# Kernel optimization log

Measured on AMD Instinct MI355X. Metric: run time of the kernel, lower is better.

The kernel has to match this reference:

```python
import jax, jax.numpy as jnp
import numpy as np

NFFT = 512
SHIFT = 160
EPS = 1e-07
LOG10 = float(np.log(10.0))


def setup_inputs() -> dict:
    key = jax.random.key(0)
    x = jax.random.normal(key, (32, 1, 96512), dtype=jnp.float32)
    n = np.arange(NFFT)
    ang = 2.0 * np.pi * np.outer(n, n) / NFFT  # [k, n]
    W_real = np.cos(ang).astype(np.float32)
    W_imag = (-np.sin(ang)).astype(np.float32)
    return {"x": x, "W_real": jnp.asarray(W_real), "W_imag": jnp.asarray(W_imag)}


def reference(x, W_real, W_imag):
    # x: [B, C, T]; W_real/W_imag: [nfft, nfft] DFT basis (kernel k over taps n)
    B, C, T = x.shape
    n_frames = (T - NFFT) // SHIFT + 1
    # strided frame extraction == Conv1d(stride=SHIFT, kernel=NFFT) unfolding
    idx = jnp.arange(n_frames)[:, None] * SHIFT + jnp.arange(NFFT)[None, :]  # [F, N]
    frames = x[:, :, idx]  # [B, C, F, N]
    real = jnp.einsum('bcfn,kn->bckf', frames, W_real)  # [B, C, nfft, F]
    imag = jnp.einsum('bcfn,kn->bckf', frames, W_imag)
    # mode == 'log': log10 of magnitude spectrogram (with epsilon inside sqrt)
    fft = jnp.log(jnp.sqrt(real * real + imag * imag + EPS)) / LOG10
    fft = fft[:, :, : NFFT // 2, :]  # keep lower half of spectrum
    # normalize_feature: zero-mean, unit-std over frequency axis (biased std)
    mean = jnp.mean(fft, axis=2, keepdims=True)
    std = jnp.std(fft, axis=2, keepdims=True)
    return (fft - mean) / (std + EPS)
```

## Files before the change

### kernel.cpp

```cpp
#include <hip/hip_runtime.h>
#include <stdint.h>

#define TLEN    96512
#define NBATCH  32
#define KOUT    256
#define SHIFT   160
#define NFRAMES 601
#define FT      76
#define NTILES  8
#define NKS     16
#define DEPTH   3
#define EPSF    1e-7f

typedef _Float16 f16;
typedef _Float16 half8 __attribute__((ext_vector_type(8)));
typedef float f32x16 __attribute__((ext_vector_type(16)));

#define SPAN       ((FT - 1) * SHIFT + 256)
#define UNITS      (SPAN / 8)
#define PLANE_B    24576
#define LDS_RED    104704
#define LDS_STAT   (LDS_RED + 6144)
#define LDS_TOTAL  (LDS_STAT + 768)

__global__ __launch_bounds__(256) void split_w_kernel(
    const float* __restrict__ Wr, const float* __restrict__ Wi,
    f16* __restrict__ wsW)
{
    int id = blockIdx.x * 256 + threadIdx.x;
    int n8 = id & 31;
    int k  = (id >> 5) & 255;
    int ri = (id >> 13) & 1;
    const float* src = (ri ? Wi : Wr) + k * 512 + n8 * 8;
    f16 h[8], l[8];
    #pragma unroll
    for (int j = 0; j < 8; ++j) {
        float v = src[j];
        h[j] = (f16)v;
        l[j] = (f16)(v - (float)h[j]);
    }
    int par = k & 1, kk = k >> 1;
    int l31 = kk & 31, J = kk >> 5;
    int ks  = n8 >> 1, lhi = n8 & 1;
    int c0  = ((par * 4 + J) * 16 + ks) * 4 + ri * 2;
    size_t off = (size_t)(l31 * 2 + lhi) * 8;
    *(half8*)(wsW + (size_t)(c0 + 0) * 512 + off) = *(half8*)h;
    *(half8*)(wsW + (size_t)(c0 + 1) * 512 + off) = *(half8*)l;
}

__device__ __forceinline__ void load_a(half8 (&a)[2][2],
    const f16* __restrict__ wsW, int par, int J, int laneoff, int ks)
{
    #pragma unroll
    for (int ri = 0; ri < 2; ++ri)
      #pragma unroll
      for (int hl = 0; hl < 2; ++hl) {
          int c = ((par * 4 + J) * 16 + ks) * 4 + ri * 2 + hl;
          a[ri][hl] = *(const half8*)(wsW + (size_t)c * 512 + laneoff);
      }
}

__device__ __forceinline__ void load_b(half8 (&bb)[3][2],
    const char* smem, int par, int l31, int lhi, int ks)
{
    #pragma unroll
    for (int nf = 0; nf < 3; ++nf)
      #pragma unroll
      for (int hl = 0; hl < 2; ++hl) {
          int u  = (nf * 32 + l31) * 20 + ks * 2 + lhi;
          int up = u ^ ((u >> 3) & 7);
          bb[nf][hl] = *(const half8*)(smem + (par * 2 + hl) * PLANE_B + up * 16);
      }
}

__device__ __forceinline__ void do_mfma(f32x16 (&acc)[3][2],
    const half8 (&a)[2][2], const half8 (&bb)[3][2])
{
    __builtin_amdgcn_s_setprio(1);
    #pragma unroll
    for (int nf = 0; nf < 3; ++nf)
      #pragma unroll
      for (int ri = 0; ri < 2; ++ri) {
          acc[nf][ri] = __builtin_amdgcn_mfma_f32_32x32x16_f16(
              a[ri][0], bb[nf][0], acc[nf][ri], 0, 0, 0);
          acc[nf][ri] = __builtin_amdgcn_mfma_f32_32x32x16_f16(
              a[ri][0], bb[nf][1], acc[nf][ri], 0, 0, 0);
          acc[nf][ri] = __builtin_amdgcn_mfma_f32_32x32x16_f16(
              a[ri][1], bb[nf][0], acc[nf][ri], 0, 0, 0);
      }
    __builtin_amdgcn_s_setprio(0);
}

__global__ __launch_bounds__(512, 2) void dft_mfma_kernel(
    const f16* __restrict__ wsW, const float* __restrict__ x,
    float* __restrict__ out)
{
    __shared__ uint4 smem4[LDS_TOTAL / 16];
    char* smem = (char*)smem4;

    const int tid  = threadIdx.x;
    const int lane = tid & 63;
    const int w    = tid >> 6;
    const int l31  = lane & 31;
    const int lhi  = lane >> 5;
    const int b    = blockIdx.y;
    const int f0   = blockIdx.x * FT;
    const int par  = w & 1;
    const int J    = w >> 1;
    const int laneoff = (l31 * 2 + lhi) * 8;

    half8 A[DEPTH][2][2];
    #pragma unroll
    for (int s = 0; s < DEPTH; ++s)
        load_a(A[s], wsW, par, J, laneoff, s);

    {
        const float* __restrict__ xb = x + (size_t)b * TLEN;
        const int t0 = f0 * SHIFT;
        for (int u = tid; u < UNITS; u += 512) {
            int t = t0 + u * 8;
            float va[8], vb[8];
            if (t + 264 <= TLEN) {
                float4 p0 = *(const float4*)(xb + t);
                float4 p1 = *(const float4*)(xb + t + 4);
                float4 q0 = *(const float4*)(xb + t + 256);
                float4 q1 = *(const float4*)(xb + t + 260);
                va[0]=p0.x; va[1]=p0.y; va[2]=p0.z; va[3]=p0.w;
                va[4]=p1.x; va[5]=p1.y; va[6]=p1.z; va[7]=p1.w;
                vb[0]=q0.x; vb[1]=q0.y; vb[2]=q0.z; vb[3]=q0.w;
                vb[4]=q1.x; vb[5]=q1.y; vb[6]=q1.z; vb[7]=q1.w;
            } else {
                #pragma unroll
                for (int j = 0; j < 8; ++j) {
                    int ta = t + j, tb = t + 256 + j;
                    va[j] = (ta < TLEN) ? xb[ta] : 0.f;
                    vb[j] = (tb < TLEN) ? xb[tb] : 0.f;
                }
            }
            f16 eh[8], el[8], oh[8], ol[8];
            #pragma unroll
            for (int j = 0; j < 8; ++j) {
                float E = va[j] + vb[j], O = va[j] - vb[j];
                eh[j] = (f16)E; el[j] = (f16)(E - (float)eh[j]);
                oh[j] = (f16)O; ol[j] = (f16)(O - (float)oh[j]);
            }
            int up = u ^ ((u >> 3) & 7);
            *(half8*)(smem + 0 * PLANE_B + up * 16) = *(half8*)eh;
            *(half8*)(smem + 1 * PLANE_B + up * 16) = *(half8*)el;
            *(half8*)(smem + 2 * PLANE_B + up * 16) = *(half8*)oh;
            *(half8*)(smem + 3 * PLANE_B + up * 16) = *(half8*)ol;
        }
    }
    __syncthreads();

    f32x16 acc[3][2] = {};

    #pragma unroll
    for (int ks = 0; ks < NKS; ++ks) {
        half8 bb[3][2];
        load_b(bb, smem, par, l31, lhi, ks);
        do_mfma(acc, A[ks % DEPTH], bb);
        if (ks + DEPTH < NKS)
            load_a(A[ks % DEPTH], wsW, par, J, laneoff, ks + DEPTH);
    }

    const float C = 0.15051499783199057f;
    float s1[3] = {0.f, 0.f, 0.f}, s2[3] = {0.f, 0.f, 0.f};
    #pragma unroll
    for (int nf = 0; nf < 3; ++nf)
      #pragma unroll
      for (int r = 0; r < 16; ++r) {
          float re = acc[nf][0][r], im = acc[nf][1][r];
          float lv = C * __log2f(re * re + im * im + EPSF);
          acc[nf][0][r] = lv;
          s1[nf] += lv;
          s2[nf] += lv * lv;
      }
    #pragma unroll
    for (int nf = 0; nf < 3; ++nf) {
        s1[nf] += __shfl_xor(s1[nf], 32);
        s2[nf] += __shfl_xor(s2[nf], 32);
    }
    float2* red = (float2*)(smem + LDS_RED);
    if (lane < 32) {
        #pragma unroll
        for (int nf = 0; nf < 3; ++nf)
            red[(w * 3 + nf) * 32 + l31] = make_float2(s1[nf], s2[nf]);
    }
    __syncthreads();
    float* stat = (float*)(smem + LDS_STAT);
    if (tid < 96) {
        float S1 = 0.f, S2 = 0.f;
        int nf = tid >> 5, c = tid & 31;
        #pragma unroll
        for (int ww = 0; ww < 8; ++ww) {
            float2 p = red[(ww * 3 + nf) * 32 + c];
            S1 += p.x; S2 += p.y;
        }
        float mean = S1 * (1.f / 256.f);
        float var  = fmaxf(S2 * (1.f / 256.f) - mean * mean, 0.f);
        stat[tid]      = mean;
        stat[96 + tid] = 1.f / (__builtin_sqrtf(var) + EPSF);
    }
    __syncthreads();

    float* patch = (float*)smem + w * (32 * 96);
    #pragma unroll
    for (int nf = 0; nf < 3; ++nf) {
        int fl = nf * 32 + l31;
        float mean = stat[fl], rstd = stat[96 + fl];
        #pragma unroll
        for (int r = 0; r < 16; ++r) {
            int kloc = (r & 3) + 8 * (r >> 2) + 4 * lhi;
            patch[kloc * 96 + fl] = (acc[nf][0][r] - mean) * rstd;
        }
    }
    #pragma unroll 8
    for (int kloc = 0; kloc < 32; ++kloc) {
        int kg = 2 * (J * 32 + kloc) + par;
        float* dst = out + ((size_t)b * KOUT + kg) * NFRAMES + f0;
        float v0 = patch[kloc * 96 + lane];
        if (f0 + lane < NFRAMES)
            dst[lane] = v0;
        if (lane < FT - 64 && f0 + 64 + lane < NFRAMES) {
            float v1 = patch[kloc * 96 + 64 + lane];
            dst[64 + lane] = v1;
        }
    }
}

extern "C" void kernel_launch(void* const* d_in, const int* in_sizes, int n_in,
                              void* d_out, int out_size, void* d_ws, size_t ws_size,
                              hipStream_t stream) {
    const float* x  = (const float*)d_in[0];
    const float* Wr = (const float*)d_in[1];
    const float* Wi = (const float*)d_in[2];
    float* out = (float*)d_out;

    f16* wsW = (f16*)d_ws;

    split_w_kernel<<<64, 256, 0, stream>>>(Wr, Wi, wsW);

    dim3 grid(NTILES, NBATCH);
    dft_mfma_kernel<<<grid, 512, 0, stream>>>(wsW, x, out);
}
```

Baseline: 35.68 us.

## Stage DFT weight fragments through LDS via direct global-to-LDS loads

Replaces the three-deep register prefetch of the fp16 hi/lo DFT weight fragments with per-wave `global_load_lds` transfers into a dedicated LDS region. Each k-step waits for the staged weights, reads them and the signal fragments from LDS, then issues the next step's weight transfer before the MFMAs. The weight layout is reordered so that lane i maps directly to its 16-byte slot. This frees VGPRs and moves weight traffic onto the LDS path, but it enlarges LDS use, shortens prefetch distance to one step, and adds full vmcnt/lgkmcnt waits on every iteration, which can expose global latency.

```diff
diff --git a/kernel.cpp b/kernel.cpp
--- a/kernel.cpp
+++ b/kernel.cpp
@@ -9,7 +9,6 @@
 #define FT      76
 #define NTILES  8
 #define NKS     16
-#define DEPTH   3
 #define EPSF    1e-7f
 
 typedef _Float16 f16;
@@ -18,8 +17,10 @@
 
 #define SPAN       ((FT - 1) * SHIFT + 256)
 #define UNITS      (SPAN / 8)
+#define A_OFF      0
+#define B_OFF      32768
 #define PLANE_B    24576
-#define LDS_RED    104704
+#define LDS_RED    137536
 #define LDS_STAT   (LDS_RED + 6144)
 #define LDS_TOTAL  (LDS_STAT + 768)
 
@@ -43,21 +44,34 @@
     int l31 = kk & 31, J = kk >> 5;
     int ks  = n8 >> 1, lhi = n8 & 1;
     int c0  = ((par * 4 + J) * 16 + ks) * 4 + ri * 2;
-    size_t off = (size_t)(l31 * 2 + lhi) * 8;
+    size_t off = (size_t)(lhi * 32 + l31) * 8;
     *(half8*)(wsW + (size_t)(c0 + 0) * 512 + off) = *(half8*)h;
     *(half8*)(wsW + (size_t)(c0 + 1) * 512 + off) = *(half8*)l;
 }
 
-__device__ __forceinline__ void load_a(half8 (&a)[2][2],
-    const f16* __restrict__ wsW, int par, int J, int laneoff, int ks)
+typedef const __attribute__((address_space(1))) uint32_t g_u32;
+typedef __attribute__((address_space(3))) uint32_t      l_u32;
+
+__device__ __forceinline__ void stage_a(const f16* __restrict__ wsW, char* smem,
+                                        int w, int lane, int par, int J, int ks)
+{
+    const f16* g = wsW + (size_t)(((par * 4 + J) * 16 + ks) * 4) * 512 + lane * 8;
+    char* lp = smem + A_OFF + w * 4096;
+    #pragma unroll
+    for (int i = 0; i < 4; ++i)
+        __builtin_amdgcn_global_load_lds((g_u32*)(g + i * 512),
+                                         (l_u32*)(lp + i * 1024), 16, 0, 0);
+}
+
+__device__ __forceinline__ void read_a(half8 (&a)[2][2], const char* smem,
+                                       int w, int lane)
 {
     #pragma unroll
     for (int ri = 0; ri < 2; ++ri)
       #pragma unroll
-      for (int hl = 0; hl < 2; ++hl) {
-          int c = ((par * 4 + J) * 16 + ks) * 4 + ri * 2 + hl;
-          a[ri][hl] = *(const half8*)(wsW + (size_t)c * 512 + laneoff);
-      }
+      for (int hl = 0; hl < 2; ++hl)
+          a[ri][hl] = *(const half8*)(smem + A_OFF + w * 4096
+                                      + (ri * 2 + hl) * 1024 + lane * 16);
 }
 
 __device__ __forceinline__ void load_b(half8 (&bb)[3][2],
@@ -69,7 +83,8 @@
       for (int hl = 0; hl < 2; ++hl) {
           int u  = (nf * 32 + l31) * 20 + ks * 2 + lhi;
           int up = u ^ ((u >> 3) & 7);
-          bb[nf][hl] = *(const half8*)(smem + (par * 2 + hl) * PLANE_B + up * 16);
+          bb[nf][hl] = *(const half8*)(smem + B_OFF + (par * 2 + hl) * PLANE_B
+                                       + up * 16);
       }
 }
 
@@ -107,12 +122,8 @@
     const int f0   = blockIdx.x * FT;
     const int par  = w & 1;
     const int J    = w >> 1;
-    const int laneoff = (l31 * 2 + lhi) * 8;
-
-    half8 A[DEPTH][2][2];
-    #pragma unroll
-    for (int s = 0; s < DEPTH; ++s)
-        load_a(A[s], wsW, par, J, laneoff, s);
+
+    stage_a(wsW, smem, w, lane, par, J, 0);
 
     {
         const float* __restrict__ xb = x + (size_t)b * TLEN;
@@ -145,10 +156,10 @@
                 oh[j] = (f16)O; ol[j] = (f16)(O - (float)oh[j]);
             }
             int up = u ^ ((u >> 3) & 7);
-            *(half8*)(smem + 0 * PLANE_B + up * 16) = *(half8*)eh;
-            *(half8*)(smem + 1 * PLANE_B + up * 16) = *(half8*)el;
-            *(half8*)(smem + 2 * PLANE_B + up * 16) = *(half8*)oh;
-            *(half8*)(smem + 3 * PLANE_B + up * 16) = *(half8*)ol;
+            *(half8*)(smem + B_OFF + 0 * PLANE_B + up * 16) = *(half8*)eh;
+            *(half8*)(smem + B_OFF + 1 * PLANE_B + up * 16) = *(half8*)el;
+            *(half8*)(smem + B_OFF + 2 * PLANE_B + up * 16) = *(half8*)oh;
+            *(half8*)(smem + B_OFF + 3 * PLANE_B + up * 16) = *(half8*)ol;
         }
     }
     __syncthreads();
@@ -157,11 +168,14 @@
 
     #pragma unroll
     for (int ks = 0; ks < NKS; ++ks) {
-        half8 bb[3][2];
+        asm volatile("s_waitcnt vmcnt(0)" ::: "memory");
+        half8 a[2][2], bb[3][2];
+        read_a(a, smem, w, lane);
         load_b(bb, smem, par, l31, lhi, ks);
-        do_mfma(acc, A[ks % DEPTH], bb);
-        if (ks + DEPTH < NKS)
-            load_a(A[ks % DEPTH], wsW, par, J, laneoff, ks + DEPTH);
+        asm volatile("s_waitcnt lgkmcnt(0)" ::: "memory");
+        if (ks + 1 < NKS)
+            stage_a(wsW, smem, w, lane, par, J, ks + 1);
+        do_mfma(acc, a, bb);
     }
 
     const float C = 0.15051499783199057f;
```

Result: slower. 38.88 us (+9.0%).
